# Performance work log

Hardware: AMD Instinct MI355X
Metric: run time of the kernel (lower is better)

Reference implementation:

```python
import jax, jax.numpy as jnp
import numpy as np

N_EMBD = 1024
N_HEAD = 16
HEAD_DIM = N_EMBD // N_HEAD


def setup_inputs() -> dict:
    key = jax.random.key(0)
    kx, kq, kk, kv, ko = jax.random.split(key, 5)
    s = 1.0 / np.sqrt(N_EMBD)
    return {
        "x": jax.random.normal(kx, (4, 2048, N_EMBD), dtype=jnp.float32),
        "Wq": jax.random.normal(kq, (N_EMBD, N_EMBD), dtype=jnp.float32) * s,
        "Wk": jax.random.normal(kk, (N_EMBD, N_EMBD), dtype=jnp.float32) * s,
        "Wv": jax.random.normal(kv, (N_EMBD, N_EMBD), dtype=jnp.float32) * s,
        "Wo": jax.random.normal(ko, (N_EMBD, N_EMBD), dtype=jnp.float32) * s,
    }


def reference(x, Wq, Wk, Wv, Wo):
    B, T, C = x.shape
    H, D = N_HEAD, HEAD_DIM
    # projections; torch Linear computes x @ W.T
    q = (x @ Wq.T).reshape(B, T, H, D).transpose(0, 2, 1, 3)  # [B,H,T,D]
    k = (x @ Wk.T).reshape(B, T, H, D).transpose(0, 2, 1, 3)
    v = (x @ Wv.T).reshape(B, T, H, D).transpose(0, 2, 1, 3)
    scores = jnp.einsum("bhtd,bhsd->bhts", q, k) / np.sqrt(D).astype(np.float32)
    causal = jnp.tril(jnp.ones((T, T), dtype=bool))
    scores = jnp.where(causal, scores, -jnp.inf)
    attn = jax.nn.softmax(scores, axis=-1)
    out = jnp.einsum("bhts,bhsd->bhtd", attn, v)  # [B,H,T,D]
    out = out.transpose(0, 2, 1, 3).reshape(B, T, C)
    return out @ Wo.T
```

## Files before the change

### kernel.cpp

```cpp
#include <hip/hip_runtime.h>
#include <hip/hip_bf16.h>


typedef __bf16 bf16_t;
typedef __bf16 bf16x4 __attribute__((ext_vector_type(4)));
typedef __bf16 bf16x8 __attribute__((ext_vector_type(8)));
typedef float  f32x4  __attribute__((ext_vector_type(4)));

#define MFMA16(a, b, c) __builtin_amdgcn_mfma_f32_16x16x32_bf16(a, b, c, 0, 0, 0)

__device__ __forceinline__ float exp2_(float x) {
#if __has_builtin(__builtin_amdgcn_exp2f)
    return __builtin_amdgcn_exp2f(x);
#else
    return __expf(x * 0.6931471805599453f);
#endif
}

__device__ __forceinline__ void gload_lds16(const bf16_t* g, bf16_t* l) {
    __builtin_amdgcn_global_load_lds(
        (const __attribute__((address_space(1))) void*)g,
        (__attribute__((address_space(3))) void*)l, 16, 0, 0);
}

__global__ __launch_bounds__(256)
void cast_all(const float* __restrict__ x,  const float* __restrict__ Wq,
              const float* __restrict__ Wk, const float* __restrict__ Wv,
              const float* __restrict__ Wo,
              bf16_t* __restrict__ xb, bf16_t* __restrict__ wqkv,
              bf16_t* __restrict__ wob) {
    int i = blockIdx.x * 256 + threadIdx.x;
    const float* src;
    bf16_t* dst;
    if (blockIdx.y == 0) {
        src = x; dst = xb;
    } else {
        if (i >= 524288) return;
        int wsel = i >> 17;
        int loc  = i & 131071;
        src = wsel == 0 ? Wq : wsel == 1 ? Wk : wsel == 2 ? Wv : Wo;
        dst = wsel == 3 ? wob : wqkv + (size_t)wsel * 1048576;
        i = loc;
    }
    const float4* p = (const float4*)src;
    float4 a = p[i * 2], b = p[i * 2 + 1];
    bf16x8 o;
    o[0] = (bf16_t)a.x; o[1] = (bf16_t)a.y; o[2] = (bf16_t)a.z; o[3] = (bf16_t)a.w;
    o[4] = (bf16_t)b.x; o[5] = (bf16_t)b.y; o[6] = (bf16_t)b.z; o[7] = (bf16_t)b.w;
    *(bf16x8*)(dst + (size_t)i * 8) = o;
}

template<int OUT_BF16>
__global__ __launch_bounds__(256)
void gemm_bt64(const bf16_t* __restrict__ A, const bf16_t* __restrict__ B,
               void* __restrict__ Cv, int M, int N, int K) {
    __shared__ bf16_t As[128 * 64];
    __shared__ bf16_t Bs[128 * 64];
    const int tid = threadIdx.x;
    const int lane = tid & 63;
    const int w = tid >> 6;
    const int wm = w >> 1, wn = w & 1;
    const int g = lane >> 4, c = lane & 15;
    const long bm = (long)blockIdx.x * 128;
    const long bn = (long)blockIdx.y * 128;

    f32x4 acc[4][4] = {};

    const int srow = tid >> 3;
    const int scb  = tid & 7;
    bf16_t* AsW = As + tid * 8;
    bf16_t* BsW = Bs + tid * 8;

    for (int k0 = 0; k0 < K; k0 += 64) {
        #pragma unroll
        for (int r = 0; r < 4; ++r) {
            int row = r * 32 + srow;
            int lb  = scb ^ (row & 7);
            gload_lds16(A + (bm + row) * (long)K + k0 + lb * 8, AsW + r * 2048);
            gload_lds16(B + (bn + row) * (long)K + k0 + lb * 8, BsW + r * 2048);
        }
        __syncthreads();
        bf16x8 bfr[4][2];
        #pragma unroll
        for (int n = 0; n < 4; ++n) {
            const int row = wn * 64 + n * 16 + c;
            #pragma unroll
            for (int ks = 0; ks < 2; ++ks)
                bfr[n][ks] = *(const bf16x8*)(Bs + row * 64 +
                                 (((ks * 4 + g) ^ (row & 7)) * 8));
        }
        #pragma unroll
        for (int m = 0; m < 4; ++m) {
            const int row = wm * 64 + m * 16 + c;
            bf16x8 af0 = *(const bf16x8*)(As + row * 64 + ((g       ^ (row & 7)) * 8));
            bf16x8 af1 = *(const bf16x8*)(As + row * 64 + (((4 + g) ^ (row & 7)) * 8));
            #pragma unroll
            for (int n = 0; n < 4; ++n) {
                acc[m][n] = MFMA16(af0, bfr[n][0], acc[m][n]);
                acc[m][n] = MFMA16(af1, bfr[n][1], acc[m][n]);
            }
        }
        __syncthreads();
    }
    #pragma unroll
    for (int m = 0; m < 4; ++m)
        #pragma unroll
        for (int n = 0; n < 4; ++n)
            #pragma unroll
            for (int i = 0; i < 4; ++i) {
                long row = bm + wm * 64 + m * 16 + g * 4 + i;
                long col = bn + wn * 64 + n * 16 + c;
                float v = acc[m][n][i];
                if (OUT_BF16) ((bf16_t*)Cv)[row * N + col] = (bf16_t)v;
                else          ((float*)Cv)[row * N + col]  = v;
            }
}

template<int OUT_BF16>
__global__ __launch_bounds__(256)
void gemm_bt(const bf16_t* __restrict__ A, const bf16_t* __restrict__ B,
             void* __restrict__ Cv, int M, int N, int K) {
    __shared__ bf16_t As[128 * 32];
    __shared__ bf16_t Bs[128 * 32];
    const int tid = threadIdx.x;
    const int lane = tid & 63;
    const int w = tid >> 6;
    const int wm = w >> 1, wn = w & 1;
    const int g = lane >> 4, c = lane & 15;
    const long bm = (long)blockIdx.x * 128;
    const long bn = (long)blockIdx.y * 128;

    f32x4 acc[4][4] = {};

    const int srow = tid >> 2;
    const int scol = (tid & 3) << 3;
    const bf16_t* Ag = A + (bm + srow) * (long)K + scol;
    const bf16_t* Bg = B + (bn + srow) * (long)K + scol;
    bf16_t* AsW = As + tid * 8;
    bf16_t* BsW = Bs + tid * 8;

    for (int k0 = 0; k0 < K; k0 += 32) {
        gload_lds16(Ag + k0,                 AsW);
        gload_lds16(Ag + k0 + (long)64 * K,  AsW + 2048);
        gload_lds16(Bg + k0,                 BsW);
        gload_lds16(Bg + k0 + (long)64 * K,  BsW + 2048);
        __syncthreads();
        bf16x8 af[4], bfr[4];
        #pragma unroll
        for (int m = 0; m < 4; ++m)
            af[m] = *(const bf16x8*)(As + (wm * 64 + m * 16 + c) * 32 + g * 8);
        #pragma unroll
        for (int n = 0; n < 4; ++n)
            bfr[n] = *(const bf16x8*)(Bs + (wn * 64 + n * 16 + c) * 32 + g * 8);
        #pragma unroll
        for (int m = 0; m < 4; ++m)
            #pragma unroll
            for (int n = 0; n < 4; ++n)
                acc[m][n] = MFMA16(af[m], bfr[n], acc[m][n]);
        __syncthreads();
    }
    #pragma unroll
    for (int m = 0; m < 4; ++m)
        #pragma unroll
        for (int n = 0; n < 4; ++n)
            #pragma unroll
            for (int i = 0; i < 4; ++i) {
                long row = bm + wm * 64 + m * 16 + g * 4 + i;
                long col = bn + wn * 64 + n * 16 + c;
                float v = acc[m][n][i];
                if (OUT_BF16) ((bf16_t*)Cv)[row * N + col] = (bf16_t)v;
                else          ((float*)Cv)[row * N + col]  = v;
            }
}


__device__ __forceinline__ void stage_K(const bf16_t* Kp, long rowb, int kb, int hcol,
                                        bf16_t* Kbuf, int tid) {
    int row = tid >> 3;
    int lb  = (tid & 7) ^ (row & 7);
    gload_lds16(Kp + (rowb + kb + row) * 3072 + hcol + lb * 8, Kbuf + tid * 8);
}

__device__ __forceinline__ bf16x8 load_V8(const bf16_t* Vp, long rowb, int kb,
                                          int hcol, int tid) {
    const int d  = tid & 63;
    const int k0 = (tid >> 6) * 8;
    bf16x8 v;
    #pragma unroll
    for (int j = 0; j < 8; ++j)
        v[j] = Vp[(rowb + kb + k0 + j) * 3072 + hcol + d];
    return v;
}

__device__ __forceinline__ void write_V8(bf16_t* Vbuf, int tid, bf16x8 v) {
    const int d  = tid & 63;
    const int k0 = (tid >> 6) * 8;
    *(bf16x8*)&Vbuf[d * 72 + k0] = v;
}

__global__ __launch_bounds__(512, 6)
void attn_kernel(const bf16_t* __restrict__ Qp, const bf16_t* __restrict__ Kp,
                 const bf16_t* __restrict__ Vp, bf16_t* __restrict__ O) {
    __shared__ bf16_t Ks[2][64 * 64];
    __shared__ bf16_t Vts[2][64 * 72];
    __shared__ bf16_t PW[8][16 * 72];

    const int tid = threadIdx.x, lane = tid & 63, w = tid >> 6;
    const int g = lane >> 4, c = lane & 15;
    const int bh = blockIdx.x;
    const int b = bh >> 4, h = bh & 15;
    const long rowb = (long)b * 2048;
    const int hcol = h * 64;
    const float QSCL = 0.18033688011112042f;

    const int q0  = 15 - blockIdx.y;
    const int qlo = q0 * 128 + w * 16;
    const int nkt = 2 * q0 + 2;

    bf16x8 qf[2];
    #pragma unroll
    for (int ks = 0; ks < 2; ++ks) {
        qf[ks] = *(const bf16x8*)(Qp + (rowb + qlo + c) * 3072 +
                                  hcol + ks * 32 + g * 8);
        #pragma unroll
        for (int j = 0; j < 8; ++j)
            qf[ks][j] = (bf16_t)((float)qf[ks][j] * QSCL);
    }

    float m_r = -1e30f;
    float l_r = 0.f;
    f32x4 acc[4] = {};

    stage_K(Kp, rowb, 0, hcol, Ks[0], tid);
    write_V8(Vts[0], tid, load_V8(Vp, rowb, 0, hcol, tid));
    __syncthreads();

    for (int t = 0; t < nkt; ++t) {
        const int cur = t & 1;
        const int kb = t * 64;
        const bool pre = (t + 1 < nkt);
        bf16x8 vreg;
        if (pre) {
            stage_K(Kp, rowb, kb + 64, hcol, Ks[cur ^ 1], tid);
            vreg = load_V8(Vp, rowb, kb + 64, hcol, tid);
        }

        if (kb <= qlo + 15) {
            f32x4 sacc[4] = {};
            __builtin_amdgcn_s_setprio(1);
            #pragma unroll
            for (int nt = 0; nt < 4; ++nt) {
                const int row = nt * 16 + c;
                #pragma unroll
                for (int ks = 0; ks < 2; ++ks) {
                    bf16x8 kf = *(const bf16x8*)&Ks[cur][row * 64 +
                                    (((ks * 4 + g) ^ (c & 7)) * 8)];
                    sacc[nt] = MFMA16(kf, qf[ks], sacc[nt]);
                }
            }
            __builtin_amdgcn_s_setprio(0);
            if (kb + 63 > qlo) {
                const int q = qlo + c;
                #pragma unroll
                for (int nt = 0; nt < 4; ++nt)
                    #pragma unroll
                    for (int i = 0; i < 4; ++i) {
                        int key = kb + nt * 16 + g * 4 + i;
                        if (key > q) sacc[nt][i] = -1e30f;
                    }
            }

            float m0 = fmaxf(fmaxf(sacc[0][0], sacc[0][1]),
                             fmaxf(fmaxf(sacc[0][2], sacc[0][3]), sacc[1][0]));
            float m1 = fmaxf(fmaxf(sacc[1][1], sacc[1][2]),
                             fmaxf(fmaxf(sacc[1][3], sacc[2][0]), sacc[2][1]));
            float m2 = fmaxf(fmaxf(sacc[2][2], sacc[2][3]),
                             fmaxf(fmaxf(sacc[3][0], sacc[3][1]),
                                   fmaxf(sacc[3][2], sacc[3][3])));
            float mx = fmaxf(fmaxf(m0, m1), m2);
            if (__any(mx > m_r + 8.f)) {
                mx = fmaxf(mx, __shfl_xor(mx, 16, 64));
                mx = fmaxf(mx, __shfl_xor(mx, 32, 64));
                float mnew = fmaxf(m_r, mx);
                float scl = exp2_(m_r - mnew);
                #pragma unroll
                for (int nt = 0; nt < 4; ++nt)
                    acc[nt] *= scl;
                l_r *= scl;
                m_r = mnew;
            }
            float rsn[4];
            #pragma unroll
            for (int nt = 0; nt < 4; ++nt) {
                #pragma unroll
                for (int i = 0; i < 4; ++i)
                    sacc[nt][i] = exp2_(sacc[nt][i] - m_r);
                rsn[nt] = (sacc[nt][0] + sacc[nt][1]) + (sacc[nt][2] + sacc[nt][3]);
            }
            l_r += (rsn[0] + rsn[1]) + (rsn[2] + rsn[3]);

            #pragma unroll
            for (int nt = 0; nt < 4; ++nt) {
                bf16x4 t4;
                #pragma unroll
                for (int i = 0; i < 4; ++i) t4[i] = (bf16_t)sacc[nt][i];
                *(bf16x4*)&PW[w][c * 72 + nt * 16 + g * 4] = t4;
            }

            __builtin_amdgcn_s_setprio(1);
            #pragma unroll
            for (int ks = 0; ks < 2; ++ks) {
                bf16x8 pf = *(const bf16x8*)&PW[w][c * 72 + ks * 32 + g * 8];
                #pragma unroll
                for (int nt = 0; nt < 4; ++nt) {
                    bf16x8 vf = *(const bf16x8*)&Vts[cur][(nt * 16 + c) * 72 +
                                                          ks * 32 + g * 8];
                    acc[nt] = MFMA16(vf, pf, acc[nt]);
                }
            }
            __builtin_amdgcn_s_setprio(0);
        }

        if (pre) write_V8(Vts[cur ^ 1], tid, vreg);
        __syncthreads();
    }

    l_r += __shfl_xor(l_r, 16, 64);
    l_r += __shfl_xor(l_r, 32, 64);
    {
        float rl = __builtin_amdgcn_rcpf(l_r);
        #pragma unroll
        for (int nt = 0; nt < 4; ++nt) {
            bf16x4 t4;
            #pragma unroll
            for (int i = 0; i < 4; ++i) t4[i] = (bf16_t)(acc[nt][i] * rl);
            *(bf16x4*)&PW[w][c * 72 + nt * 16 + g * 4] = t4;
        }
    }
    #pragma unroll
    for (int p = 0; p < 2; ++p) {
        int row = p * 8 + (lane >> 3);
        int ch  = (lane & 7) * 8;
        bf16x8 v = *(const bf16x8*)&PW[w][row * 72 + ch];
        *(bf16x8*)&O[(rowb + qlo + row) * 1024 + hcol + ch] = v;
    }
}

extern "C" void kernel_launch(void* const* d_in, const int* in_sizes, int n_in,
                              void* d_out, int out_size, void* d_ws, size_t ws_size,
                              hipStream_t stream) {
    const float* x  = (const float*)d_in[0];
    const float* Wq = (const float*)d_in[1];
    const float* Wk = (const float*)d_in[2];
    const float* Wv = (const float*)d_in[3];
    const float* Wo = (const float*)d_in[4];

    const int M = 8192;
    const int C = 1024;

    char* ws = (char*)d_ws;
    bf16_t* xb   = (bf16_t*)(ws);
    bf16_t* wqkv = (bf16_t*)(ws + ((size_t)16 << 20));
    bf16_t* wob  = (bf16_t*)(ws + ((size_t)22 << 20));
    bf16_t* qkv  = (bf16_t*)(ws + ((size_t)24 << 20));
    bf16_t* aob  = (bf16_t*)(ws + ((size_t)72 << 20));

    cast_all<<<dim3(4096, 2), 256, 0, stream>>>(x, Wq, Wk, Wv, Wo, xb, wqkv, wob);

    gemm_bt64<1><<<dim3(M / 128, 3072 / 128), 256, 0, stream>>>(xb, wqkv, qkv, M, 3072, C);

    attn_kernel<<<dim3(64, 16), 512, 0, stream>>>(
        qkv, qkv + 1024, qkv + 2048, aob);

    gemm_bt<0><<<dim3(M / 128, C / 128), 256, 0, stream>>>(aob, wob, d_out, M, C, C);
}
```

Before: 173.9 us.

## Add 256x256 eight-phase pipelined GEMM for QKV projection, use bt64 for output projection

Adds a new 512-thread GEMM kernel with 256x256 tiles, double-buffered swizzled LDS and an eight-phase schedule. Each phase interleaves a half-tile global-to-LDS load with MFMA work, using explicit vmcnt waits, barriers and setprio, and it replaces the 128x128 gemm_bt64 for the QKV projection. The output projection moves from the K=32-step gemm_bt to gemm_bt64, and the old gemm_bt is removed. The aim is to hide load latency and raise data reuse per tile, at the cost of 128KB of LDS and high register pressure. With only 32x12 blocks on the grid, occupancy may be limited.

```diff
diff --git a/kernel.cpp b/kernel.cpp
--- a/kernel.cpp
+++ b/kernel.cpp
@@ -50,6 +50,112 @@
     *(bf16x8*)(dst + (size_t)i * 8) = o;
 }
 
+__device__ __forceinline__ void mfma16x(f32x4 (*acc)[4], int m0,
+                                        bf16x8 a00, bf16x8 a01,
+                                        bf16x8 a10, bf16x8 a11,
+                                        const bf16x8 bfr[4][2]) {
+    #pragma unroll
+    for (int n = 0; n < 4; ++n) {
+        acc[m0][n]     = MFMA16(a00, bfr[n][0], acc[m0][n]);
+        acc[m0][n]     = MFMA16(a01, bfr[n][1], acc[m0][n]);
+        acc[m0 + 1][n] = MFMA16(a10, bfr[n][0], acc[m0 + 1][n]);
+        acc[m0 + 1][n] = MFMA16(a11, bfr[n][1], acc[m0 + 1][n]);
+    }
+}
+
+__global__ __launch_bounds__(512, 2)
+void gemm_8ph(const bf16_t* __restrict__ A, const bf16_t* __restrict__ B,
+              bf16_t* __restrict__ C, int M, int N, int K) {
+    __shared__ bf16_t sm[2][2][256 * 64];
+    const int tid = threadIdx.x;
+    const int lane = tid & 63, w = tid >> 6;
+    const int wr = w >> 2, wc = w & 3;
+    const int g = lane >> 4, c = lane & 15;
+    const long bm = (long)blockIdx.x * 256;
+    const long bn = (long)blockIdx.y * 256;
+
+    const int srow8 = tid >> 3;
+    const int pb = tid & 7;
+
+    auto STAGE_H = [&](int buf, int op, int h, int kt) {
+        const bf16_t* base = op ? B + bn * (long)K : A + bm * (long)K;
+        #pragma unroll
+        for (int r = 0; r < 2; ++r) {
+            int row = h * 128 + r * 64 + srow8;
+            int lb  = pb ^ (row & 7);
+            gload_lds16(base + (long)row * K + kt * 64 + lb * 8,
+                        &sm[buf][op][row * 64 + pb * 8]);
+        }
+    };
+    auto LDA = [&](int buf, int m, int k) -> bf16x8 {
+        int row = wr * 128 + m * 16 + c;
+        return *(const bf16x8*)&sm[buf][0][row * 64 + (((k * 4 + g) ^ (row & 7)) * 8)];
+    };
+    auto LDB = [&](int buf, int n, int k) -> bf16x8 {
+        int row = wc * 64 + n * 16 + c;
+        return *(const bf16x8*)&sm[buf][1][row * 64 + (((k * 4 + g) ^ (row & 7)) * 8)];
+    };
+
+#define PHASE(BUF, M0, ISSUE_STMT, WAIT_STMT)                          \
+    {                                                                  \
+        bf16x8 a00 = LDA(BUF, M0, 0),     a01 = LDA(BUF, M0, 1);       \
+        bf16x8 a10 = LDA(BUF, M0 + 1, 0), a11 = LDA(BUF, M0 + 1, 1);   \
+        ISSUE_STMT;                                                    \
+        WAIT_STMT;                                                     \
+        __builtin_amdgcn_s_barrier();                                  \
+        asm volatile("s_waitcnt lgkmcnt(0)" ::: "memory");             \
+        __builtin_amdgcn_sched_barrier(0);                             \
+        __builtin_amdgcn_s_setprio(1);                                 \
+        mfma16x(acc, M0, a00, a01, a10, a11, bfr);                     \
+        __builtin_amdgcn_s_setprio(0);                                 \
+        __builtin_amdgcn_s_barrier();                                  \
+    }
+
+    f32x4 acc[8][4] = {};
+    bf16x8 bfr[4][2];
+    const int NJ = K / 128;
+
+    STAGE_H(0, 1, 0, 0); STAGE_H(0, 1, 1, 0);
+    STAGE_H(0, 0, 0, 0); STAGE_H(0, 0, 1, 0);
+    STAGE_H(1, 1, 0, 1); STAGE_H(1, 1, 1, 1);
+    asm volatile("s_waitcnt vmcnt(4)" ::: "memory");
+    __builtin_amdgcn_s_barrier();
+
+    for (int j = 0; j < NJ; ++j) {
+        const int t0 = 2 * j;
+        const bool more = (j + 1 < NJ);
+
+        #pragma unroll
+        for (int n = 0; n < 4; ++n) { bfr[n][0] = LDB(0, n, 0); bfr[n][1] = LDB(0, n, 1); }
+        PHASE(0, 0, STAGE_H(1, 0, 0, t0 + 1), (void)0);
+        PHASE(0, 2, STAGE_H(1, 0, 1, t0 + 1), (void)0);
+        PHASE(0, 4, if (more) STAGE_H(0, 1, 0, t0 + 2), (void)0);
+        PHASE(0, 6, if (more) STAGE_H(0, 1, 1, t0 + 2),
+              if (more) { asm volatile("s_waitcnt vmcnt(4)" ::: "memory"); }
+              else      { asm volatile("s_waitcnt vmcnt(0)" ::: "memory"); });
+
+        #pragma unroll
+        for (int n = 0; n < 4; ++n) { bfr[n][0] = LDB(1, n, 0); bfr[n][1] = LDB(1, n, 1); }
+        PHASE(1, 0, if (more) STAGE_H(0, 0, 0, t0 + 2), (void)0);
+        PHASE(1, 2, if (more) STAGE_H(0, 0, 1, t0 + 2), (void)0);
+        PHASE(1, 4, if (more) STAGE_H(1, 1, 0, t0 + 3), (void)0);
+        PHASE(1, 6, if (more) STAGE_H(1, 1, 1, t0 + 3),
+              if (more) { asm volatile("s_waitcnt vmcnt(4)" ::: "memory"); });
+    }
+#undef PHASE
+
+    #pragma unroll
+    for (int m = 0; m < 8; ++m)
+        #pragma unroll
+        for (int n = 0; n < 4; ++n)
+            #pragma unroll
+            for (int i = 0; i < 4; ++i) {
+                long row = bm + wr * 128 + m * 16 + g * 4 + i;
+                long col = bn + wc * 64 + n * 16 + c;
+                C[row * N + col] = (bf16_t)acc[m][n][i];
+            }
+}
+
 template<int OUT_BF16>
 __global__ __launch_bounds__(256)
 void gemm_bt64(const bf16_t* __restrict__ A, const bf16_t* __restrict__ B,
@@ -116,64 +222,6 @@
             }
 }
 
-template<int OUT_BF16>
-__global__ __launch_bounds__(256)
-void gemm_bt(const bf16_t* __restrict__ A, const bf16_t* __restrict__ B,
-             void* __restrict__ Cv, int M, int N, int K) {
-    __shared__ bf16_t As[128 * 32];
-    __shared__ bf16_t Bs[128 * 32];
-    const int tid = threadIdx.x;
-    const int lane = tid & 63;
-    const int w = tid >> 6;
-    const int wm = w >> 1, wn = w & 1;
-    const int g = lane >> 4, c = lane & 15;
-    const long bm = (long)blockIdx.x * 128;
-    const long bn = (long)blockIdx.y * 128;
-
-    f32x4 acc[4][4] = {};
-
-    const int srow = tid >> 2;
-    const int scol = (tid & 3) << 3;
-    const bf16_t* Ag = A + (bm + srow) * (long)K + scol;
-    const bf16_t* Bg = B + (bn + srow) * (long)K + scol;
-    bf16_t* AsW = As + tid * 8;
-    bf16_t* BsW = Bs + tid * 8;
-
-    for (int k0 = 0; k0 < K; k0 += 32) {
-        gload_lds16(Ag + k0,                 AsW);
-        gload_lds16(Ag + k0 + (long)64 * K,  AsW + 2048);
-        gload_lds16(Bg + k0,                 BsW);
-        gload_lds16(Bg + k0 + (long)64 * K,  BsW + 2048);
-        __syncthreads();
-        bf16x8 af[4], bfr[4];
-        #pragma unroll
-        for (int m = 0; m < 4; ++m)
-            af[m] = *(const bf16x8*)(As + (wm * 64 + m * 16 + c) * 32 + g * 8);
-        #pragma unroll
-        for (int n = 0; n < 4; ++n)
-            bfr[n] = *(const bf16x8*)(Bs + (wn * 64 + n * 16 + c) * 32 + g * 8);
-        #pragma unroll
-        for (int m = 0; m < 4; ++m)
-            #pragma unroll
-            for (int n = 0; n < 4; ++n)
-                acc[m][n] = MFMA16(af[m], bfr[n], acc[m][n]);
-        __syncthreads();
-    }
-    #pragma unroll
-    for (int m = 0; m < 4; ++m)
-        #pragma unroll
-        for (int n = 0; n < 4; ++n)
-            #pragma unroll
-            for (int i = 0; i < 4; ++i) {
-                long row = bm + wm * 64 + m * 16 + g * 4 + i;
-                long col = bn + wn * 64 + n * 16 + c;
-                float v = acc[m][n][i];
-                if (OUT_BF16) ((bf16_t*)Cv)[row * N + col] = (bf16_t)v;
-                else          ((float*)Cv)[row * N + col]  = v;
-            }
-}
-
-
 __device__ __forceinline__ void stage_K(const bf16_t* Kp, long rowb, int kb, int hcol,
                                         bf16_t* Kbuf, int tid) {
     int row = tid >> 3;
@@ -367,10 +415,10 @@
 
     cast_all<<<dim3(4096, 2), 256, 0, stream>>>(x, Wq, Wk, Wv, Wo, xb, wqkv, wob);
 
-    gemm_bt64<1><<<dim3(M / 128, 3072 / 128), 256, 0, stream>>>(xb, wqkv, qkv, M, 3072, C);
+    gemm_8ph<<<dim3(M / 256, 3072 / 256), 512, 0, stream>>>(xb, wqkv, qkv, M, 3072, C);
 
     attn_kernel<<<dim3(64, 16), 512, 0, stream>>>(
         qkv, qkv + 1024, qkv + 2048, aob);
 
-    gemm_bt<0><<<dim3(M / 128, C / 128), 256, 0, stream>>>(aob, wob, d_out, M, C, C);
-}
+    gemm_bt64<0><<<dim3(M / 128, C / 128), 256, 0, stream>>>(aob, wob, d_out, M, C, C);
+}
```

Result: faster. 165.1 us (-5.1%).
